# Optimization experiments

Measured on AMD Instinct MI355X. Metric: run time of the kernel, lower is better.

## Reference

```python
import jax, jax.numpy as jnp
import numpy as np

B, S, D, H, DQ, DM = 1, 2048, 1024, 16, 64, 4096
EPS = 1e-5
TEMPERATURE = 1.0


def layer_norm(x, gamma, beta):
    m = x.mean(-1, keepdims=True)
    v = jnp.mean((x - m) ** 2, axis=-1, keepdims=True)  # unbiased=False
    return gamma * (x - m) / jnp.sqrt(v + EPS) + beta


def setup_inputs() -> dict:
    key = jax.random.key(0)
    ks = jax.random.split(key, 12)
    w = lambda k, shape: jax.random.normal(k, shape, jnp.float32) * 0.02
    return {
        "E": jax.random.normal(ks[0], (B, S, D), jnp.float32),
        "mask": jnp.tril(jnp.ones((S, S), jnp.int32)),  # causal
        "W_Q": w(ks[1], (D, D)),
        "W_K": w(ks[2], (D, D)),
        "W_V": w(ks[3], (D, D)),
        "W_O": w(ks[4], (D, D)),
        "H_Q": w(ks[5], (H, DQ, D)),  # per-head Linear weights [out,in]
        "H_K": w(ks[6], (H, DQ, D)),
        "H_V": w(ks[7], (H, DQ, D)),
        "L1_w": w(ks[8], (DM, D)),
        "L1_b": jnp.zeros((DM,), jnp.float32),
        "L2_w": w(ks[9], (D, DM)),
        "L2_b": jnp.zeros((D,), jnp.float32),
        "gamma1": jnp.ones((D,), jnp.float32),
        "beta1": jnp.zeros((D,), jnp.float32),
        "gamma2": jnp.ones((D,), jnp.float32),
        "beta2": jnp.zeros((D,), jnp.float32),
    }


def reference(E, mask, W_Q, W_K, W_V, W_O, H_Q, H_K, H_V,
              L1_w, L1_b, L2_w, L2_b, gamma1, beta1, gamma2, beta2):
    # --- multi-head attention (dropout omitted: inference/eval) ---
    Q = E @ W_Q.T  # [B,S,D]
    K = E @ W_K.T
    V = E @ W_V.T
    # per-head projections (vectorized over the torch per-head Linear loop)
    q = jnp.einsum('bsd,hed->bhse', Q, H_Q)  # [B,H,S,DQ]
    k = jnp.einsum('bsd,hed->bhse', K, H_K)
    v = jnp.einsum('bsd,hed->bhse', V, H_V)
    scores = jnp.einsum('bhse,bhte->bhst', q, k) / jnp.sqrt(jnp.float32(DQ))
    scores = jnp.where(mask == 0, jnp.float32(-1e9), scores)
    weights = jax.nn.softmax(scores, axis=-1) / TEMPERATURE
    o = jnp.einsum('bhst,bhte->bhse', weights, v)        # [B,H,S,DQ]
    o = o.transpose(0, 2, 1, 3).reshape(E.shape[0], E.shape[1], D)  # concat heads
    att = o @ W_O.T
    # residual 1: E + Norm(sublayer(E))  (norm applied to sublayer output)
    x1 = E + layer_norm(att, gamma1, beta1)
    # --- MLP ---
    mlp = jax.nn.relu(x1 @ L1_w.T + L1_b) @ L2_w.T + L2_b
    return x1 + layer_norm(mlp, gamma2, beta2)
```

## Files before the change

kernel.cpp:

```cpp
#include <hip/hip_runtime.h>
#include <hip/hip_bf16.h>
#include <stdint.h>
#include <stddef.h>

typedef __attribute__((ext_vector_type(8))) short bf16x8;
typedef __attribute__((ext_vector_type(4))) short short4v;
typedef __attribute__((ext_vector_type(4))) float f32x4;

#define DEV static __device__ __forceinline__

DEV float bf2f(short s) {
  union { unsigned int u; float f; } c;
  c.u = ((unsigned int)(unsigned short)s) << 16;
  return c.f;
}
DEV short f2bf(float f) {
  union { float f; unsigned int u; } c; c.f = f;
  c.u += 0x7fffu + ((c.u >> 16) & 1);
  return (short)(c.u >> 16);
}
DEV unsigned int cvtpk_bf16(float lo, float hi) {
  unsigned int r;
  asm("v_cvt_pk_bf16_f32 %0, %1, %2" : "=v"(r) : "v"(lo), "v"(hi));
  return r;
}

struct CvtJob { const float* src; short* dst; int n4; };
struct CvtArgs { CvtJob j[10]; };

__global__ __launch_bounds__(256) void cvt_kernel(CvtArgs a) {
  int tid = blockIdx.x * blockDim.x + threadIdx.x;
  int stride = gridDim.x * blockDim.x;
  for (int jj = 0; jj < 10; ++jj) {
    const float4* s = (const float4*)a.j[jj].src;
    short4v* d = (short4v*)a.j[jj].dst;
    int n4 = a.j[jj].n4;
    for (int i = tid; i < n4; i += stride) {
      float4 v = s[i];
      short4v o = { f2bf(v.x), f2bf(v.y), f2bf(v.z), f2bf(v.w) };
      d[i] = o;
    }
  }
}

struct GemmArgs {
  const short* A[4];
  const short* B[4];
  void* C[4];
  const float* bias;
  int M, N, K, klen, kbase_step;
};

template<int EPI>
__global__ __launch_bounds__(256) void gemm_bt(GemmArgs g) {
  __shared__ alignas(16) short As[128 * 64];
  __shared__ alignas(16) short Bs[128 * 64];
  int z = blockIdx.z;
  const short* A = g.A[z];
  const short* B = g.B[z];
  int kb = z * g.kbase_step;

  int bx = blockIdx.x, by = blockIdx.y;
  int tid = threadIdx.x;
  int lane = tid & 63, wid = tid >> 6;
  int l15 = lane & 15, l4 = lane >> 4;
  int wr = (wid >> 1) * 64, wc = (wid & 1) * 64;
  int K = g.K, N = g.N;

  const short* Ab = A + (size_t)(by * 128) * K + kb;
  const short* Bb = B + (size_t)(bx * 128) * K + kb;

  int sR = lane >> 3;
  int sC = ((lane & 7) ^ sR) * 8;

  f32x4 acc[4][4] = {};

  for (int k0 = 0; k0 < g.klen; k0 += 64) {
    __syncthreads();
    const short* Abk = Ab + k0;
    const short* Bbk = Bb + k0;
    #pragma unroll
    for (int i = 0; i < 4; ++i) {
      int rbase = (wid * 4 + i) * 8;
      __builtin_amdgcn_global_load_lds(
          (const __attribute__((address_space(1))) void*)(Abk + (size_t)(rbase + sR) * K + sC),
          (__attribute__((address_space(3))) void*)&As[rbase * 64], 16, 0, 0);
      __builtin_amdgcn_global_load_lds(
          (const __attribute__((address_space(1))) void*)(Bbk + (size_t)(rbase + sR) * K + sC),
          (__attribute__((address_space(3))) void*)&Bs[rbase * 64], 16, 0, 0);
    }
    __syncthreads();

    bf16x8 af[2][4], bfr[2][4];
    int rj = l15 & 7;
    #pragma unroll
    for (int kk = 0; kk < 2; ++kk) {
      #pragma unroll
      for (int mi = 0; mi < 4; ++mi) {
        int r = wr + mi * 16 + l15;
        af[kk][mi] = *(const bf16x8*)&As[r * 64 + (((kk << 2) | l4) ^ rj) * 8];
      }
      #pragma unroll
      for (int ni = 0; ni < 4; ++ni) {
        int r = wc + ni * 16 + l15;
        bfr[kk][ni] = *(const bf16x8*)&Bs[r * 64 + (((kk << 2) | l4) ^ rj) * 8];
      }
    }
    #pragma unroll
    for (int kk = 0; kk < 2; ++kk)
      #pragma unroll
      for (int mi = 0; mi < 4; ++mi)
        #pragma unroll
        for (int ni = 0; ni < 4; ++ni)
          acc[mi][ni] = __builtin_amdgcn_mfma_f32_16x16x32_bf16(af[kk][mi], bfr[kk][ni], acc[mi][ni], 0, 0, 0);
  }

  #pragma unroll
  for (int mi = 0; mi < 4; ++mi) {
    #pragma unroll
    for (int ni = 0; ni < 4; ++ni) {
      int col = bx * 128 + wc + ni * 16 + l15;
      float bv = 0.f;
      if (EPI == 1) bv = g.bias[col];
      bool ct = (EPI == 3) || (EPI == 4 && z == 2);
      if (ct) {
        int row0 = by * 128 + wr + mi * 16 + l4 * 4;
        short4v o4 = { f2bf(acc[mi][ni][0]), f2bf(acc[mi][ni][1]),
                       f2bf(acc[mi][ni][2]), f2bf(acc[mi][ni][3]) };
        *(short4v*)&((short*)g.C[z])[(size_t)col * g.M + row0] = o4;
      } else {
        #pragma unroll
        for (int j = 0; j < 4; ++j) {
          int row = by * 128 + wr + mi * 16 + l4 * 4 + j;
          float v = acc[mi][ni][j];
          if (EPI == 0 || EPI == 4) {
            ((short*)g.C[z])[(size_t)row * N + col] = f2bf(v);
          } else if (EPI == 1) {
            v = fmaxf(v + bv, 0.f);
            ((short*)g.C[z])[(size_t)row * N + col] = f2bf(v);
          } else {
            ((float*)g.C[z])[(size_t)row * N + col] = v;
          }
        }
      }
    }
  }
}

__global__ __launch_bounds__(256, 4) void flash_attn(
    const short* __restrict__ q, const short* __restrict__ k,
    const short* __restrict__ vt, short* __restrict__ o,
    float* __restrict__ Opart, float* __restrict__ Ml)
{
  const int HD = 1024, SS = 2048;
  int h = blockIdx.x;
  int cid = blockIdx.y;
  int qb = 0, cx = cid;
  while (cx >= (qb >> 3) + 1) { cx -= (qb >> 3) + 1; ++qb; }
  int nch = (qb >> 3) + 1;
  int tf = cx << 3;
  int tl = min(qb, tf + 7);
  int qbase = qb << 6;

  int tid = threadIdx.x;
  int wid = tid >> 6, lane = tid & 63;
  int l15 = lane & 15, l4 = lane >> 4;

  __shared__ alignas(16) short Ks[2][64 * 64];
  __shared__ alignas(16) short Vs[2][64 * 64];
  __shared__ alignas(16) char PsB[4][2048];

  bf16x8 qf[2];
  {
    int qr = qbase + wid * 16 + l15;
    const short* qp = q + (size_t)qr * HD + h * 64 + l4 * 8;
    bf16x8 r0 = *(const bf16x8*)qp;
    bf16x8 r1 = *(const bf16x8*)(qp + 32);
    const float SC = 0.1803368801f;
    #pragma unroll
    for (int j = 0; j < 8; ++j) {
      qf[0][j] = f2bf(bf2f(r0[j]) * SC);
      qf[1][j] = f2bf(bf2f(r1[j]) * SC);
    }
  }

  int sR = lane >> 3;
  int sC = (lane & 7) ^ sR;

  auto stage = [&](int buf, int t0) {
    const short* kbase = k + (size_t)t0 * HD + h * 64;
    const short* vbase = vt + (size_t)(h * 64) * SS + t0;
    #pragma unroll
    for (int i = 0; i < 2; ++i) {
      int rb = wid * 16 + i * 8;
      __builtin_amdgcn_global_load_lds(
          (const __attribute__((address_space(1))) void*)(kbase + (size_t)(rb + sR) * HD + sC * 8),
          (__attribute__((address_space(3))) void*)&Ks[buf][rb * 64], 16, 0, 0);
      __builtin_amdgcn_global_load_lds(
          (const __attribute__((address_space(1))) void*)(vbase + (size_t)(rb + sR) * SS + sC * 8),
          (__attribute__((address_space(3))) void*)&Vs[buf][rb * 64], 16, 0, 0);
    }
  };

  f32x4 oacc[4] = {};
  float mrun = -1e30f, lrun = 0.f;
  int q_g = qbase + wid * 16 + l15;
  int sbase = (lane & 48) + ((lane & 48) >> 2);

  char* Pw = &PsB[wid][l15 << 7];
  int swz = (l15 & 7) << 4;

  stage(0, tf << 6);
  __syncthreads();
  int cur = 0;

  for (int tt = tf; tt <= tl; ++tt) {
    if (tt < tl) stage(cur ^ 1, (tt + 1) << 6);

    const short* KsB = &Ks[cur][0];
    const short* VsB = &Vs[cur][0];
    int t0 = tt << 6;

    f32x4 sc[4] = {};
    __builtin_amdgcn_s_setprio(1);
    #pragma unroll
    for (int ks = 0; ks < 2; ++ks)
      #pragma unroll
      for (int ns = 0; ns < 4; ++ns) {
        int r = ns * 16 + l15;
        bf16x8 kf = *(const bf16x8*)&KsB[r * 64 + (((ks << 2) | l4) ^ (r & 7)) * 8];
        sc[ns] = __builtin_amdgcn_mfma_f32_16x16x32_bf16(kf, qf[ks], sc[ns], 0, 0, 0);
      }
    __builtin_amdgcn_s_setprio(0);

    if (tt == qb) {
      #pragma unroll
      for (int ns = 0; ns < 4; ++ns)
        #pragma unroll
        for (int j = 0; j < 4; ++j) {
          int t_g = t0 + ns * 16 + l4 * 4 + j;
          if (t_g > q_g) sc[ns][j] = -1e30f;
        }
    }

    float mloc = sc[0][0];
    #pragma unroll
    for (int ns = 0; ns < 4; ++ns)
      #pragma unroll
      for (int j = 0; j < 4; ++j) mloc = fmaxf(mloc, sc[ns][j]);
    mloc = fmaxf(mloc, __shfl_xor(mloc, 16, 64));
    mloc = fmaxf(mloc, __shfl_xor(mloc, 32, 64));

    if (!__all(mloc - mrun <= 8.0f)) {
      float mnew = fmaxf(mrun, mloc);
      float sco = exp2f(mrun - mnew);
      float scR[4];
      #pragma unroll
      for (int j = 0; j < 4; ++j) scR[j] = __shfl(sco, sbase + j, 64);
      #pragma unroll
      for (int es = 0; es < 4; ++es)
        #pragma unroll
        for (int j = 0; j < 4; ++j) oacc[es][j] *= scR[j];
      lrun *= sco;
      mrun = mnew;
    }

    float psum = 0.f;
    float p[4][4];
    #pragma unroll
    for (int ns = 0; ns < 4; ++ns)
      #pragma unroll
      for (int j = 0; j < 4; ++j) {
        p[ns][j] = exp2f(sc[ns][j] - mrun);
        psum += p[ns][j];
      }
    psum += __shfl_xor(psum, 16, 64);
    psum += __shfl_xor(psum, 32, 64);
    lrun += psum;

    #pragma unroll
    for (int ns = 0; ns < 4; ++ns) {
      uint2 pv = { cvtpk_bf16(p[ns][0], p[ns][1]), cvtpk_bf16(p[ns][2], p[ns][3]) };
      *(uint2*)&Pw[((ns << 5) | (l4 << 3)) ^ swz] = pv;
    }

    __builtin_amdgcn_s_setprio(1);
    #pragma unroll
    for (int ks = 0; ks < 2; ++ks) {
      bf16x8 pf = *(const bf16x8*)&Pw[((ks << 6) | (l4 << 4)) ^ swz];
      #pragma unroll
      for (int es = 0; es < 4; ++es) {
        int r = es * 16 + l15;
        bf16x8 vf = *(const bf16x8*)&VsB[r * 64 + (((ks << 2) | l4) ^ (r & 7)) * 8];
        oacc[es] = __builtin_amdgcn_mfma_f32_16x16x32_bf16(pf, vf, oacc[es], 0, 0, 0);
      }
    }
    __builtin_amdgcn_s_setprio(0);

    __syncthreads();
    cur ^= 1;
  }

  if (nch == 1) {
    float linv = 1.f / lrun;
    float invR[4];
    #pragma unroll
    for (int j = 0; j < 4; ++j) invR[j] = __shfl(linv, sbase + j, 64);
    #pragma unroll
    for (int es = 0; es < 4; ++es)
      #pragma unroll
      for (int j = 0; j < 4; ++j) {
        int row = qbase + wid * 16 + l4 * 4 + j;
        o[(size_t)row * HD + h * 64 + es * 16 + l15] = f2bf(oacc[es][j] * invR[j]);
      }
  } else {
    size_t slot = (size_t)h * 80 + cid;
    float* op = Opart + slot * 4096;
    #pragma unroll
    for (int es = 0; es < 4; ++es)
      #pragma unroll
      for (int j = 0; j < 4; ++j) {
        int row = wid * 16 + l4 * 4 + j;
        op[row * 64 + es * 16 + l15] = oacc[es][j];
      }
    if (l4 == 0) {
      Ml[slot * 128 + wid * 16 + l15] = mrun;
      Ml[slot * 128 + 64 + wid * 16 + l15] = lrun;
    }
  }
}

__global__ __launch_bounds__(256) void attn_combine(
    const float* __restrict__ Opart, const float* __restrict__ Ml,
    short* __restrict__ o)
{
  const int HD = 1024;
  int h = blockIdx.x;
  int qb = 8 + blockIdx.y;
  int nch = (qb >> 3) + 1;
  int cb = 0;
  for (int qq = 0; qq < qb; ++qq) cb += (qq >> 3) + 1;
  int tid = threadIdx.x;
  int r = tid >> 2;
  int cq = (tid & 3) << 4;
  size_t slot0 = (size_t)h * 80 + cb;

  float mk[4], lk[4];
  float M = -1e30f;
  #pragma unroll
  for (int kk = 0; kk < 4; ++kk) {
    bool en = kk < nch;
    mk[kk] = en ? Ml[(slot0 + kk) * 128 + r] : -1e30f;
    lk[kk] = en ? Ml[(slot0 + kk) * 128 + 64 + r] : 0.f;
    M = fmaxf(M, mk[kk]);
  }
  float L = 0.f, w[4];
  #pragma unroll
  for (int kk = 0; kk < 4; ++kk) { w[kk] = exp2f(mk[kk] - M); L += w[kk] * lk[kk]; }

  float acc[16] = {};
  #pragma unroll
  for (int kk = 0; kk < 4; ++kk) {
    if (kk < nch) {
      const float* op = Opart + (slot0 + kk) * 4096 + r * 64 + cq;
      float wk = w[kk];
      #pragma unroll
      for (int c4 = 0; c4 < 4; ++c4) {
        float4 v = *(const float4*)&op[c4 * 4];
        acc[c4 * 4 + 0] += wk * v.x;
        acc[c4 * 4 + 1] += wk * v.y;
        acc[c4 * 4 + 2] += wk * v.z;
        acc[c4 * 4 + 3] += wk * v.w;
      }
    }
  }
  float inv = 1.f / L;
  int orow = (qb << 6) + r;
  short* dst = o + (size_t)orow * HD + h * 64 + cq;
  #pragma unroll
  for (int c4 = 0; c4 < 4; ++c4) {
    short4v ov = { f2bf(acc[c4 * 4 + 0] * inv), f2bf(acc[c4 * 4 + 1] * inv),
                   f2bf(acc[c4 * 4 + 2] * inv), f2bf(acc[c4 * 4 + 3] * inv) };
    *(short4v*)&dst[c4 * 4] = ov;
  }
}

__global__ __launch_bounds__(256) void ln_res1(
    const float* __restrict__ P0, const float* __restrict__ P1,
    const float* __restrict__ E,
    const float* __restrict__ gamma, const float* __restrict__ beta,
    float* __restrict__ x1f, short* __restrict__ x1b)
{
  int row = blockIdx.x, tid = threadIdx.x;
  int lane = tid & 63, wid = tid >> 6;
  size_t idx = (size_t)row * 1024 + tid * 4;
  float4 p0 = *(const float4*)&P0[idx];
  float4 p1 = *(const float4*)&P1[idx];
  float a[4] = { p0.x + p1.x, p0.y + p1.y, p0.z + p1.z, p0.w + p1.w };
  float s = a[0] + a[1] + a[2] + a[3];
  float q = a[0]*a[0] + a[1]*a[1] + a[2]*a[2] + a[3]*a[3];
  #pragma unroll
  for (int off = 1; off < 64; off <<= 1) { s += __shfl_xor(s, off, 64); q += __shfl_xor(q, off, 64); }
  __shared__ float red[8];
  if (lane == 0) { red[wid] = s; red[4 + wid] = q; }
  __syncthreads();
  s = red[0] + red[1] + red[2] + red[3];
  q = red[4] + red[5] + red[6] + red[7];
  float mean = s * (1.f / 1024.f);
  float var = q * (1.f / 1024.f) - mean * mean;
  float rstd = rsqrtf(var + 1e-5f);
  float4 ev = *(const float4*)&E[idx];
  float4 gv = *(const float4*)&gamma[tid * 4];
  float4 bv = *(const float4*)&beta[tid * 4];
  float o0 = ev.x + gv.x * (a[0] - mean) * rstd + bv.x;
  float o1 = ev.y + gv.y * (a[1] - mean) * rstd + bv.y;
  float o2 = ev.z + gv.z * (a[2] - mean) * rstd + bv.z;
  float o3 = ev.w + gv.w * (a[3] - mean) * rstd + bv.w;
  float4 xo = { o0, o1, o2, o3 };
  *(float4*)&x1f[idx] = xo;
  short4v xb = { f2bf(o0), f2bf(o1), f2bf(o2), f2bf(o3) };
  *(short4v*)&x1b[idx] = xb;
}

__global__ __launch_bounds__(256) void ln_res2(
    const float* __restrict__ M0, const float* __restrict__ M1,
    const float* __restrict__ M2, const float* __restrict__ M3,
    const float* __restrict__ bias, const float* __restrict__ x1f,
    const float* __restrict__ gamma, const float* __restrict__ beta,
    float* __restrict__ out)
{
  int row = blockIdx.x, tid = threadIdx.x;
  int lane = tid & 63, wid = tid >> 6;
  size_t idx = (size_t)row * 1024 + tid * 4;
  float4 m0 = *(const float4*)&M0[idx];
  float4 m1 = *(const float4*)&M1[idx];
  float4 m2 = *(const float4*)&M2[idx];
  float4 m3 = *(const float4*)&M3[idx];
  float4 bb = *(const float4*)&bias[tid * 4];
  float a[4] = { m0.x + m1.x + m2.x + m3.x + bb.x,
                 m0.y + m1.y + m2.y + m3.y + bb.y,
                 m0.z + m1.z + m2.z + m3.z + bb.z,
                 m0.w + m1.w + m2.w + m3.w + bb.w };
  float s = a[0] + a[1] + a[2] + a[3];
  float q = a[0]*a[0] + a[1]*a[1] + a[2]*a[2] + a[3]*a[3];
  #pragma unroll
  for (int off = 1; off < 64; off <<= 1) { s += __shfl_xor(s, off, 64); q += __shfl_xor(q, off, 64); }
  __shared__ float red[8];
  if (lane == 0) { red[wid] = s; red[4 + wid] = q; }
  __syncthreads();
  s = red[0] + red[1] + red[2] + red[3];
  q = red[4] + red[5] + red[6] + red[7];
  float mean = s * (1.f / 1024.f);
  float var = q * (1.f / 1024.f) - mean * mean;
  float rstd = rsqrtf(var + 1e-5f);
  float4 xv = *(const float4*)&x1f[idx];
  float4 gv = *(const float4*)&gamma[tid * 4];
  float4 bv = *(const float4*)&beta[tid * 4];
  float4 ov = { xv.x + gv.x * (a[0] - mean) * rstd + bv.x,
                xv.y + gv.y * (a[1] - mean) * rstd + bv.y,
                xv.z + gv.z * (a[2] - mean) * rstd + bv.z,
                xv.w + gv.w * (a[3] - mean) * rstd + bv.w };
  *(float4*)&out[idx] = ov;
}

extern "C" void kernel_launch(void* const* d_in, const int* in_sizes, int n_in,
                              void* d_out, int out_size, void* d_ws, size_t ws_size,
                              hipStream_t stream)
{
  (void)in_sizes; (void)n_in; (void)out_size;
  const int S = 2048, D = 1024, DM = 4096, H = 16;
  const size_t MB = 1u << 20;
  const float* E   = (const float*)d_in[0];
  const float* W_Q = (const float*)d_in[2];
  const float* W_K = (const float*)d_in[3];
  const float* W_V = (const float*)d_in[4];
  const float* W_O = (const float*)d_in[5];
  const float* H_Q = (const float*)d_in[6];
  const float* H_K = (const float*)d_in[7];
  const float* H_V = (const float*)d_in[8];
  const float* L1w = (const float*)d_in[9];
  const float* L1b = (const float*)d_in[10];
  const float* L2w = (const float*)d_in[11];
  const float* L2b = (const float*)d_in[12];
  const float* g1  = (const float*)d_in[13];
  const float* b1  = (const float*)d_in[14];
  const float* g2  = (const float*)d_in[15];
  const float* b2  = (const float*)d_in[16];

  char* base = (char*)d_ws;
  if (ws_size < 90 * MB) return;

  short* Ebf  = (short*)(base + 0 * MB);
  short* Wqb  = (short*)(base + 4 * MB);
  short* Wkb  = (short*)(base + 6 * MB);
  short* Wvb  = (short*)(base + 8 * MB);
  short* Wob  = (short*)(base + 10 * MB);
  short* Hqb  = (short*)(base + 12 * MB);
  short* Hkb  = (short*)(base + 14 * MB);
  short* Hvb  = (short*)(base + 16 * MB);
  short* L1wb = (short*)(base + 18 * MB);
  short* L2wb = (short*)(base + 26 * MB);
  short* Qp   = (short*)(base + 34 * MB);
  short* Kp   = (short*)(base + 38 * MB);
  short* Vp   = (short*)(base + 42 * MB);
  short* qh   = (short*)(base + 46 * MB);
  short* kh   = (short*)(base + 50 * MB);
  short* vtb  = (short*)(base + 54 * MB);
  short* obuf = (short*)(base + 58 * MB);
  short* x1b  = (short*)(base + 62 * MB);
  float* x1f  = (float*)(base + 66 * MB);
  short* hbuf = (short*)(base + 74 * MB);
  float* WOP0 = (float*)(base + 74 * MB);
  float* WOP1 = (float*)(base + 82 * MB);
  float* MP0  = (float*)(base + 34 * MB);
  float* MP1  = (float*)(base + 42 * MB);
  float* MP2  = (float*)(base + 50 * MB);
  float* MP3  = (float*)(base + 58 * MB);
  float* Opart = (float*)(base + 66 * MB);
  float* Ml    = (float*)(base + 86 * MB);

  CvtArgs ca;
  ca.j[0] = { E,   Ebf,  S * D / 4 };
  ca.j[1] = { W_Q, Wqb,  D * D / 4 };
  ca.j[2] = { W_K, Wkb,  D * D / 4 };
  ca.j[3] = { W_V, Wvb,  D * D / 4 };
  ca.j[4] = { W_O, Wob,  D * D / 4 };
  ca.j[5] = { H_Q, Hqb,  D * D / 4 };
  ca.j[6] = { H_K, Hkb,  D * D / 4 };
  ca.j[7] = { H_V, Hvb,  D * D / 4 };
  ca.j[8] = { L1w, L1wb, DM * D / 4 };
  ca.j[9] = { L2w, L2wb, DM * D / 4 };
  cvt_kernel<<<2048, 256, 0, stream>>>(ca);

  GemmArgs ga;

  ga = {};
  ga.A[0] = Ebf; ga.A[1] = Ebf; ga.A[2] = Ebf;
  ga.B[0] = Wqb; ga.B[1] = Wkb; ga.B[2] = Wvb;
  ga.C[0] = Qp;  ga.C[1] = Kp;  ga.C[2] = Vp;
  ga.M = S; ga.N = D; ga.K = D; ga.klen = D; ga.kbase_step = 0;
  gemm_bt<0><<<dim3(D / 128, S / 128, 3), 256, 0, stream>>>(ga);

  ga = {};
  ga.A[0] = Qp;  ga.A[1] = Kp;  ga.A[2] = Vp;
  ga.B[0] = Hqb; ga.B[1] = Hkb; ga.B[2] = Hvb;
  ga.C[0] = qh;  ga.C[1] = kh;  ga.C[2] = vtb;
  ga.M = S; ga.N = D; ga.K = D; ga.klen = D; ga.kbase_step = 0;
  gemm_bt<4><<<dim3(D / 128, S / 128, 3), 256, 0, stream>>>(ga);

  flash_attn<<<dim3(H, 80), 256, 0, stream>>>(qh, kh, vtb, obuf, Opart, Ml);
  attn_combine<<<dim3(H, 24), 256, 0, stream>>>(Opart, Ml, obuf);

  ga = {};
  ga.A[0] = obuf; ga.A[1] = obuf;
  ga.B[0] = Wob;  ga.B[1] = Wob;
  ga.C[0] = WOP0; ga.C[1] = WOP1;
  ga.M = S; ga.N = D; ga.K = D; ga.klen = D / 2; ga.kbase_step = D / 2;
  gemm_bt<2><<<dim3(D / 128, S / 128, 2), 256, 0, stream>>>(ga);

  ln_res1<<<S, 256, 0, stream>>>(WOP0, WOP1, E, g1, b1, x1f, x1b);

  ga = {};
  ga.A[0] = x1b; ga.B[0] = L1wb; ga.C[0] = hbuf;
  ga.bias = L1b;
  ga.M = S; ga.N = DM; ga.K = D; ga.klen = D; ga.kbase_step = 0;
  gemm_bt<1><<<dim3(DM / 128, S / 128, 1), 256, 0, stream>>>(ga);

  ga = {};
  ga.A[0] = hbuf; ga.A[1] = hbuf; ga.A[2] = hbuf; ga.A[3] = hbuf;
  ga.B[0] = L2wb; ga.B[1] = L2wb; ga.B[2] = L2wb; ga.B[3] = L2wb;
  ga.C[0] = MP0;  ga.C[1] = MP1;  ga.C[2] = MP2;  ga.C[3] = MP3;
  ga.M = S; ga.N = D; ga.K = DM; ga.klen = DM / 4; ga.kbase_step = DM / 4;
  gemm_bt<2><<<dim3(D / 128, S / 128, 4), 256, 0, stream>>>(ga);

  ln_res2<<<S, 256, 0, stream>>>(MP0, MP1, MP2, MP3, L2b, x1f, g2, b2, (float*)d_out);
}
```

Measured before the change: 185.4 us.

## Precompose per-head and input projection weights; halve split-K for MLP down-projection

Uses associativity to multiply H_Q·W_Q (and likewise for K and V) into combined 1024x1024 weights. Getting a B^T-form operand needs a new transpose-convert kernel. This swaps the 2048-row Q/K/V projection GEMM for a 1024-row weight-weight GEMM, removing one activation-sized GEMM and its intermediate buffers. Separately, the L2 GEMM split-K drops from 4 to 2 partials, so less partial-sum traffic feeds the second layernorm, at the cost of fewer blocks in flight. Rounding changes because the combined weights are rounded to bf16.

```diff
diff --git a/kernel.cpp b/kernel.cpp
--- a/kernel.cpp
+++ b/kernel.cpp
@@ -26,12 +26,12 @@
 }
 
 struct CvtJob { const float* src; short* dst; int n4; };
-struct CvtArgs { CvtJob j[10]; };
+struct CvtArgs { CvtJob j[8]; int n; };
 
 __global__ __launch_bounds__(256) void cvt_kernel(CvtArgs a) {
   int tid = blockIdx.x * blockDim.x + threadIdx.x;
   int stride = gridDim.x * blockDim.x;
-  for (int jj = 0; jj < 10; ++jj) {
+  for (int jj = 0; jj < a.n; ++jj) {
     const float4* s = (const float4*)a.j[jj].src;
     short4v* d = (short4v*)a.j[jj].dst;
     int n4 = a.j[jj].n4;
@@ -40,6 +40,34 @@
       short4v o = { f2bf(v.x), f2bf(v.y), f2bf(v.z), f2bf(v.w) };
       d[i] = o;
     }
+  }
+}
+
+struct TcvtArgs { const float* src[3]; short* dst[3]; };
+
+__global__ __launch_bounds__(256) void tcvt_kernel(TcvtArgs a) {
+  __shared__ float tile[64][65];
+  int z = blockIdx.z;
+  const float* src = a.src[z];
+  short* dst = a.dst[z];
+  int bi = blockIdx.x * 64;
+  int bj = blockIdx.y * 64;
+  int t = threadIdx.x;
+  int r0 = t >> 4;
+  int c4 = (t & 15) * 4;
+  #pragma unroll
+  for (int rr = 0; rr < 4; ++rr) {
+    int r = rr * 16 + r0;
+    float4 v = *(const float4*)&src[(size_t)(bi + r) * 1024 + bj + c4];
+    tile[r][c4] = v.x; tile[r][c4 + 1] = v.y; tile[r][c4 + 2] = v.z; tile[r][c4 + 3] = v.w;
+  }
+  __syncthreads();
+  #pragma unroll
+  for (int ww = 0; ww < 4; ++ww) {
+    int orow = ww * 16 + r0;
+    short4v o = { f2bf(tile[c4][orow]), f2bf(tile[c4 + 1][orow]),
+                  f2bf(tile[c4 + 2][orow]), f2bf(tile[c4 + 3][orow]) };
+    *(short4v*)&dst[(size_t)(bj + orow) * 1024 + bi + c4] = o;
   }
 }
 
@@ -424,7 +452,6 @@
 
 __global__ __launch_bounds__(256) void ln_res2(
     const float* __restrict__ M0, const float* __restrict__ M1,
-    const float* __restrict__ M2, const float* __restrict__ M3,
     const float* __restrict__ bias, const float* __restrict__ x1f,
     const float* __restrict__ gamma, const float* __restrict__ beta,
     float* __restrict__ out)
@@ -434,13 +461,11 @@
   size_t idx = (size_t)row * 1024 + tid * 4;
   float4 m0 = *(const float4*)&M0[idx];
   float4 m1 = *(const float4*)&M1[idx];
-  float4 m2 = *(const float4*)&M2[idx];
-  float4 m3 = *(const float4*)&M3[idx];
   float4 bb = *(const float4*)&bias[tid * 4];
-  float a[4] = { m0.x + m1.x + m2.x + m3.x + bb.x,
-                 m0.y + m1.y + m2.y + m3.y + bb.y,
-                 m0.z + m1.z + m2.z + m3.z + bb.z,
-                 m0.w + m1.w + m2.w + m3.w + bb.w };
+  float a[4] = { m0.x + m1.x + bb.x,
+                 m0.y + m1.y + bb.y,
+                 m0.z + m1.z + bb.z,
+                 m0.w + m1.w + bb.w };
   float s = a[0] + a[1] + a[2] + a[3];
   float q = a[0]*a[0] + a[1]*a[1] + a[2]*a[2] + a[3]*a[3];
   #pragma unroll
@@ -491,18 +516,18 @@
   if (ws_size < 90 * MB) return;
 
   short* Ebf  = (short*)(base + 0 * MB);
-  short* Wqb  = (short*)(base + 4 * MB);
-  short* Wkb  = (short*)(base + 6 * MB);
-  short* Wvb  = (short*)(base + 8 * MB);
+  short* TWq  = (short*)(base + 4 * MB);
+  short* TWk  = (short*)(base + 6 * MB);
+  short* TWv  = (short*)(base + 8 * MB);
   short* Wob  = (short*)(base + 10 * MB);
   short* Hqb  = (short*)(base + 12 * MB);
   short* Hkb  = (short*)(base + 14 * MB);
   short* Hvb  = (short*)(base + 16 * MB);
   short* L1wb = (short*)(base + 18 * MB);
   short* L2wb = (short*)(base + 26 * MB);
-  short* Qp   = (short*)(base + 34 * MB);
-  short* Kp   = (short*)(base + 38 * MB);
-  short* Vp   = (short*)(base + 42 * MB);
+  short* Cq   = (short*)(base + 34 * MB);
+  short* Ck   = (short*)(base + 36 * MB);
+  short* Cv   = (short*)(base + 38 * MB);
   short* qh   = (short*)(base + 46 * MB);
   short* kh   = (short*)(base + 50 * MB);
   short* vtb  = (short*)(base + 54 * MB);
@@ -514,36 +539,37 @@
   float* WOP1 = (float*)(base + 82 * MB);
   float* MP0  = (float*)(base + 34 * MB);
   float* MP1  = (float*)(base + 42 * MB);
-  float* MP2  = (float*)(base + 50 * MB);
-  float* MP3  = (float*)(base + 58 * MB);
   float* Opart = (float*)(base + 66 * MB);
   float* Ml    = (float*)(base + 86 * MB);
 
   CvtArgs ca;
   ca.j[0] = { E,   Ebf,  S * D / 4 };
-  ca.j[1] = { W_Q, Wqb,  D * D / 4 };
-  ca.j[2] = { W_K, Wkb,  D * D / 4 };
-  ca.j[3] = { W_V, Wvb,  D * D / 4 };
-  ca.j[4] = { W_O, Wob,  D * D / 4 };
-  ca.j[5] = { H_Q, Hqb,  D * D / 4 };
-  ca.j[6] = { H_K, Hkb,  D * D / 4 };
-  ca.j[7] = { H_V, Hvb,  D * D / 4 };
-  ca.j[8] = { L1w, L1wb, DM * D / 4 };
-  ca.j[9] = { L2w, L2wb, DM * D / 4 };
+  ca.j[1] = { W_O, Wob,  D * D / 4 };
+  ca.j[2] = { H_Q, Hqb,  D * D / 4 };
+  ca.j[3] = { H_K, Hkb,  D * D / 4 };
+  ca.j[4] = { H_V, Hvb,  D * D / 4 };
+  ca.j[5] = { L1w, L1wb, DM * D / 4 };
+  ca.j[6] = { L2w, L2wb, DM * D / 4 };
+  ca.n = 7;
   cvt_kernel<<<2048, 256, 0, stream>>>(ca);
 
+  TcvtArgs ta;
+  ta.src[0] = W_Q; ta.src[1] = W_K; ta.src[2] = W_V;
+  ta.dst[0] = TWq; ta.dst[1] = TWk; ta.dst[2] = TWv;
+  tcvt_kernel<<<dim3(16, 16, 3), 256, 0, stream>>>(ta);
+
   GemmArgs ga;
+
+  ga = {};
+  ga.A[0] = Hqb; ga.A[1] = Hkb; ga.A[2] = Hvb;
+  ga.B[0] = TWq; ga.B[1] = TWk; ga.B[2] = TWv;
+  ga.C[0] = Cq;  ga.C[1] = Ck;  ga.C[2] = Cv;
+  ga.M = D; ga.N = D; ga.K = D; ga.klen = D; ga.kbase_step = 0;
+  gemm_bt<0><<<dim3(D / 128, D / 128, 3), 256, 0, stream>>>(ga);
 
   ga = {};
   ga.A[0] = Ebf; ga.A[1] = Ebf; ga.A[2] = Ebf;
-  ga.B[0] = Wqb; ga.B[1] = Wkb; ga.B[2] = Wvb;
-  ga.C[0] = Qp;  ga.C[1] = Kp;  ga.C[2] = Vp;
-  ga.M = S; ga.N = D; ga.K = D; ga.klen = D; ga.kbase_step = 0;
-  gemm_bt<0><<<dim3(D / 128, S / 128, 3), 256, 0, stream>>>(ga);
-
-  ga = {};
-  ga.A[0] = Qp;  ga.A[1] = Kp;  ga.A[2] = Vp;
-  ga.B[0] = Hqb; ga.B[1] = Hkb; ga.B[2] = Hvb;
+  ga.B[0] = Cq;  ga.B[1] = Ck;  ga.B[2] = Cv;
   ga.C[0] = qh;  ga.C[1] = kh;  ga.C[2] = vtb;
   ga.M = S; ga.N = D; ga.K = D; ga.klen = D; ga.kbase_step = 0;
   gemm_bt<4><<<dim3(D / 128, S / 128, 3), 256, 0, stream>>>(ga);
@@ -567,11 +593,11 @@
   gemm_bt<1><<<dim3(DM / 128, S / 128, 1), 256, 0, stream>>>(ga);
 
   ga = {};
-  ga.A[0] = hbuf; ga.A[1] = hbuf; ga.A[2] = hbuf; ga.A[3] = hbuf;
-  ga.B[0] = L2wb; ga.B[1] = L2wb; ga.B[2] = L2wb; ga.B[3] = L2wb;
-  ga.C[0] = MP0;  ga.C[1] = MP1;  ga.C[2] = MP2;  ga.C[3] = MP3;
-  ga.M = S; ga.N = D; ga.K = DM; ga.klen = DM / 4; ga.kbase_step = DM / 4;
-  gemm_bt<2><<<dim3(D / 128, S / 128, 4), 256, 0, stream>>>(ga);
-
-  ln_res2<<<S, 256, 0, stream>>>(MP0, MP1, MP2, MP3, L2b, x1f, g2, b2, (float*)d_out);
-}
+  ga.A[0] = hbuf; ga.A[1] = hbuf;
+  ga.B[0] = L2wb; ga.B[1] = L2wb;
+  ga.C[0] = MP0;  ga.C[1] = MP1;
+  ga.M = S; ga.N = D; ga.K = DM; ga.klen = DM / 2; ga.kbase_step = DM / 2;
+  gemm_bt<2><<<dim3(D / 128, S / 128, 2), 256, 0, stream>>>(ga);
+
+  ln_res2<<<S, 256, 0, stream>>>(MP0, MP1, L2b, x1f, g2, b2, (float*)d_out);
+}
```

New measurement: 196.8 us. 1.06x slower.
